# Optimization experiments

Measured on AMD Instinct MI355X. Metric: run time of the kernel, lower is better.

## Reference

```python
import jax, jax.numpy as jnp
import numpy as np

N_EMBD = 1024
N_HEAD = 16
HEAD_DIM = 64


def setup_inputs() -> dict:
    key = jax.random.key(0)
    ks = jax.random.split(key, 5)
    x = jax.random.normal(ks[0], (4, 2048, N_EMBD), dtype=jnp.float32)
    # qkv_proj: Linear(n_embd, 3*n_embd) -- torch weight is [out, in]
    W_qkv = jax.random.normal(ks[1], (3 * N_EMBD, N_EMBD), dtype=jnp.float32) * 0.02
    b_qkv = jnp.zeros((3 * N_EMBD,), dtype=jnp.float32)
    W_out = jax.random.normal(ks[2], (N_EMBD, N_EMBD), dtype=jnp.float32) * 0.02
    b_out = jnp.zeros((N_EMBD,), dtype=jnp.float32)
    return {"x": x, "W_qkv": W_qkv, "b_qkv": b_qkv, "W_out": W_out, "b_out": b_out}


def reference(x, W_qkv, b_qkv, W_out, b_out):
    B, S, C = x.shape
    scale = 1.0 / np.sqrt(HEAD_DIM)
    qkv = jnp.einsum('bsc,oc->bso', x, W_qkv) + b_qkv  # [B,S,3C]
    q, k, v = jnp.split(qkv, 3, axis=-1)
    # [B,S,C] -> [B,H,S,Dh]
    def to_heads(t):
        return t.reshape(B, S, N_HEAD, HEAD_DIM).transpose(0, 2, 1, 3)
    q, k, v = to_heads(q), to_heads(k), to_heads(v)
    scores = jnp.einsum('bhqd,bhkd->bhqk', q, k) * scale  # [B,H,S,S]
    causal = jnp.tril(jnp.ones((S, S), dtype=bool))
    scores = jnp.where(causal[None, None], scores, -jnp.inf)
    weights = jax.nn.softmax(scores.astype(jnp.float32), axis=-1).astype(q.dtype)
    y = jnp.einsum('bhqk,bhkd->bhqd', weights, v)  # [B,H,S,Dh]
    y = y.transpose(0, 2, 1, 3).reshape(B, S, C)
    return jnp.einsum('bsc,oc->bso', y, W_out) + b_out
```

## Files before the change

### kernel.cpp

```cpp
#include <hip/hip_runtime.h>
#include <stdint.h>
#include <stddef.h>

typedef __attribute__((ext_vector_type(8))) short short8;
typedef __attribute__((ext_vector_type(4))) float f32x4;
typedef __attribute__((ext_vector_type(16))) float f32x16;
typedef __attribute__((ext_vector_type(4))) unsigned short ushort4v;
typedef __attribute__((ext_vector_type(4))) unsigned int uint4v;

#define SEQ   2048
#define NH    16
#define BATCH 4
#define GK    1024

__device__ __forceinline__ unsigned short f2bf(float f) {
  union { float f; unsigned int u; } v; v.f = f;
  unsigned int u = v.u;
  u += 0x7fffu + ((u >> 16) & 1u);
  return (unsigned short)(u >> 16);
}

__device__ __forceinline__ unsigned cvtpk_bf16(float lo, float hi) {
  unsigned r;
  asm("v_cvt_pk_bf16_f32 %0, %1, %2" : "=v"(r) : "v"(lo), "v"(hi));
  return r;
}

__device__ __forceinline__ void plswap(unsigned &x, unsigned &y) {
#if __has_builtin(__builtin_amdgcn_permlane32_swap)
  auto r = __builtin_amdgcn_permlane32_swap((int)x, (int)y, false, false);
  x = (unsigned)r[0]; y = (unsigned)r[1];
#else
  const unsigned sx = (unsigned)__shfl_xor((int)x, 32);
  const unsigned sy = (unsigned)__shfl_xor((int)y, 32);
  const bool hi = (threadIdx.x & 63) >= 32;
  const unsigned nx = hi ? sy : x;
  const unsigned ny = hi ? y : sx;
  x = nx; y = ny;
#endif
}

__device__ __forceinline__ void gload16(const unsigned short* g, unsigned short* l) {
  __builtin_amdgcn_global_load_lds(
      (const __attribute__((address_space(1))) unsigned int*)g,
      (__attribute__((address_space(3))) unsigned int*)l, 16, 0, 0);
}

__global__ void cvt_all(const float* __restrict__ x, const float* __restrict__ wqkv,
                        const float* __restrict__ wout, unsigned short* __restrict__ dst) {
  const int N1 = (8192 * 1024) / 4, N2 = (3072 * 1024) / 4, N3 = (1024 * 1024) / 4;
  int i = blockIdx.x * blockDim.x + threadIdx.x;
  const int stride = gridDim.x * blockDim.x;
  for (; i < N1 + N2 + N3; i += stride) {
    float4 v;
    if (i < N1)            v = reinterpret_cast<const float4*>(x)[i];
    else if (i < N1 + N2)  v = reinterpret_cast<const float4*>(wqkv)[i - N1];
    else                   v = reinterpret_cast<const float4*>(wout)[i - N1 - N2];
    ushort4v o;
    o[0] = f2bf(v.x); o[1] = f2bf(v.y); o[2] = f2bf(v.z); o[3] = f2bf(v.w);
    reinterpret_cast<ushort4v*>(dst)[i] = o;
  }
}

template<int MODE>
__global__ __launch_bounds__(256, 3)
void gemm_bt(const unsigned short* __restrict__ A,
             const unsigned short* __restrict__ Bw,
             const float* __restrict__ bias,
             unsigned short* __restrict__ q_ws,
             unsigned short* __restrict__ k_ws,
             unsigned short* __restrict__ v_ws,
             float* __restrict__ fout,
             int N)
{
  __shared__ __attribute__((aligned(16))) unsigned short As[128 * 64];
  __shared__ __attribute__((aligned(16))) unsigned short Bs[128 * 64];

  const int t = threadIdx.x;
  const int w = t >> 6, lane = t & 63;
  const int g = lane >> 4, c = lane & 15;
  const int wrow = w >> 1, wcol = w & 1;
  const int m0 = blockIdx.y * 128;
  const int n0 = blockIdx.x * 128;

  const int r8 = lane >> 3;
  const int cgs = (lane & 7) ^ r8;

  const f32x4 fz = {0.f, 0.f, 0.f, 0.f};
  f32x4 acc[4][4];
#pragma unroll
  for (int i = 0; i < 4; ++i)
#pragma unroll
    for (int j = 0; j < 4; ++j) acc[i][j] = fz;

  for (int ks = 0; ks < GK; ks += 64) {
    __syncthreads();
#pragma unroll
    for (int i = 0; i < 4; ++i) {
      const int RB = (i * 4 + w) * 8;
      gload16(A + (size_t)(m0 + RB + r8) * GK + ks + cgs * 8, &As[RB * 64]);
      gload16(Bw + (size_t)(n0 + RB + r8) * GK + ks + cgs * 8, &Bs[RB * 64]);
    }
    __syncthreads();
#pragma unroll
    for (int kk = 0; kk < 2; ++kk) {
      short8 af[4], bfr[4];
#pragma unroll
      for (int mi = 0; mi < 4; ++mi) {
        const int row = wrow * 64 + mi * 16 + c;
        af[mi] = *reinterpret_cast<const short8*>(&As[row * 64 + (((kk * 4 + g) ^ (row & 7)) << 3)]);
      }
#pragma unroll
      for (int ni = 0; ni < 4; ++ni) {
        const int row = wcol * 64 + ni * 16 + c;
        bfr[ni] = *reinterpret_cast<const short8*>(&Bs[row * 64 + (((kk * 4 + g) ^ (row & 7)) << 3)]);
      }
#pragma unroll
      for (int mi = 0; mi < 4; ++mi)
#pragma unroll
        for (int ni = 0; ni < 4; ++ni)
          acc[mi][ni] = __builtin_amdgcn_mfma_f32_16x16x32_bf16(af[mi], bfr[ni], acc[mi][ni], 0, 0, 0);
    }
  }

  if (MODE == 0) {
    const int sec = n0 >> 10;
    unsigned short* dst = (sec == 0) ? q_ws : ((sec == 1) ? k_ws : v_ws);
    const float qsc = (sec == 0) ? (0.125f * 1.44269504f) : 1.0f;
#pragma unroll
    for (int ni = 0; ni < 4; ++ni) {
      const int n = n0 + wcol * 64 + ni * 16 + c;
      const float bb = bias[n];
      const int hh = (n & 1023) >> 6;
      const int d = n & 63;
#pragma unroll
      for (int mi = 0; mi < 4; ++mi) {
#pragma unroll
        for (int r = 0; r < 4; ++r) {
          const int m = m0 + wrow * 64 + mi * 16 + g * 4 + r;
          const int b = m >> 11, s = m & 2047;
          const float val = (acc[mi][ni][r] + bb) * qsc;
          dst[((size_t)((b * NH + hh) * SEQ + s) << 6) + d] = f2bf(val);
        }
      }
    }
  } else {
#pragma unroll
    for (int ni = 0; ni < 4; ++ni) {
      const int n = n0 + wcol * 64 + ni * 16 + c;
      const float bb = bias[n];
#pragma unroll
      for (int mi = 0; mi < 4; ++mi) {
#pragma unroll
        for (int r = 0; r < 4; ++r) {
          const int m = m0 + wrow * 64 + mi * 16 + g * 4 + r;
          fout[(size_t)m * N + n] = acc[mi][ni][r] + bb;
        }
      }
    }
  }
}

__global__ __launch_bounds__(256)
void transpose_v(const unsigned short* __restrict__ v, unsigned short* __restrict__ vt) {
  __shared__ unsigned short T[64][72];
  const int t = threadIdx.x;
  const int bh = blockIdx.y, s0 = blockIdx.x * 64;
  const unsigned short* src = v + ((size_t)bh * SEQ + s0) * 64;
#pragma unroll
  for (int rep = 0; rep < 2; ++rep) {
    const int u = rep * 256 + t;
    const int sr = u >> 3, cg = u & 7;
    const short8 x = *reinterpret_cast<const short8*>(src + (size_t)sr * 64 + cg * 8);
    *reinterpret_cast<short8*>(&T[sr][cg * 8]) = x;
  }
  __syncthreads();
  unsigned short* dst = vt + (size_t)bh * 64 * SEQ + s0;
#pragma unroll
  for (int rep = 0; rep < 2; ++rep) {
    const int u = rep * 256 + t;
    const int d = u >> 3, sc8 = u & 7;
    short8 x;
#pragma unroll
    for (int j = 0; j < 8; ++j) x[j] = (short)T[sc8 * 8 + j][d];
    *reinterpret_cast<short8*>(dst + (size_t)d * SEQ + sc8 * 8) = x;
  }
}

__global__ __launch_bounds__(512, 4)
void attn_fwd6(const unsigned short* __restrict__ q_ws,
               const unsigned short* __restrict__ k_ws,
               const unsigned short* __restrict__ vt_ws,
               unsigned short* __restrict__ y_ws)
{
  __shared__ __attribute__((aligned(16))) unsigned short Ks[2][64 * 64];
  __shared__ __attribute__((aligned(16))) unsigned short Vs[3][64 * 64];

  const int t = threadIdx.x;
  const int w = t >> 6, lane = t & 63;
  const int ql = lane & 31, hi = lane >> 5;
  const int bh = blockIdx.y, b = bh >> 4, h = bh & 15;
  const int jt = (blockIdx.y >= 32) ? (7 - (int)blockIdx.x) : (int)blockIdx.x;
  const int wq0 = jt * 256 + w * 32;
  const int nkt = 4 * jt + 4;

  const int s_row = t >> 3;
  const int s_swz = (t & 7) ^ (s_row & 7);

  const unsigned short* kbase = k_ws + (size_t)bh * SEQ * 64;
  const unsigned short* vbase = vt_ws + (size_t)bh * 64 * SEQ;

  auto stage = [&](int kt, int kb, int vb) {
    gload16(kbase + (size_t)kt * 4096 + s_row * 64 + s_swz * 8, &Ks[kb][w * 512]);
    gload16(vbase + (size_t)s_row * SEQ + kt * 64 + s_swz * 8, &Vs[vb][w * 512]);
  };

  const unsigned short* qr = q_ws + ((size_t)bh * SEQ + (wq0 + ql)) * 64;
  short8 qf[4];
#pragma unroll
  for (int ks = 0; ks < 4; ++ks)
    qf[ks] = *reinterpret_cast<const short8*>(qr + ks * 16 + hi * 8);

  f32x16 o0, o1;
#pragma unroll
  for (int i = 0; i < 16; ++i) { o0[i] = 0.f; o1[i] = 0.f; }
  float m_run = -1e30f, lsum = 0.f;
  short8 pa[4];

  stage(0, 0, 0);

#pragma unroll 1
  for (int kt = 0; kt < nkt; ++kt) {
    __syncthreads();
    if (kt + 1 < nkt) stage(kt + 1, (kt + 1) & 1, (kt + 1) % 3);
    const int cur = kt & 1;
    const int pvb = (kt + 2) % 3;
    const int kt64 = kt * 64;
    const bool act  = (kt64 <= wq0 + 31);
    const bool actp = (kt > 0) && (kt64 - 64 <= wq0 + 31);

    f32x16 s0, s1;
    if (act) {
#pragma unroll
      for (int i = 0; i < 16; ++i) { s0[i] = 0.f; s1[i] = 0.f; }
      __builtin_amdgcn_s_setprio(1);
#pragma unroll
      for (int ks = 0; ks < 4; ++ks) {
        const short8 kfl = *reinterpret_cast<const short8*>(
            &Ks[cur][ql * 64 + (((2 * ks + hi) ^ (ql & 7)) << 3)]);
        const short8 kfh = *reinterpret_cast<const short8*>(
            &Ks[cur][(32 + ql) * 64 + (((2 * ks + hi) ^ (ql & 7)) << 3)]);
        s0 = __builtin_amdgcn_mfma_f32_32x32x16_bf16(kfl, qf[ks], s0, 0, 0, 0);
        s1 = __builtin_amdgcn_mfma_f32_32x32x16_bf16(kfh, qf[ks], s1, 0, 0, 0);
      }
      __builtin_amdgcn_s_setprio(0);
    }
    if (actp) {
      __builtin_amdgcn_s_setprio(1);
#pragma unroll
      for (int ks = 0; ks < 4; ++ks) {
        const short8 vfl = *reinterpret_cast<const short8*>(
            &Vs[pvb][ql * 64 + (((2 * ks + hi) ^ (ql & 7)) << 3)]);
        const short8 vfh = *reinterpret_cast<const short8*>(
            &Vs[pvb][(32 + ql) * 64 + (((2 * ks + hi) ^ (ql & 7)) << 3)]);
        o0 = __builtin_amdgcn_mfma_f32_32x32x16_bf16(pa[ks], vfl, o0, 0, 0, 0);
        o1 = __builtin_amdgcn_mfma_f32_32x32x16_bf16(pa[ks], vfh, o1, 0, 0, 0);
      }
      __builtin_amdgcn_s_setprio(0);
    }
    if (act) {
      if (kt64 + 63 > wq0) {
        const int gq = wq0 + ql;
#pragma unroll
        for (int r = 0; r < 16; ++r) {
          const int krow = (r & 3) + 8 * (r >> 2) + 4 * hi;
          if (kt64 + krow > gq)      s0[r] = -1e30f;
          if (kt64 + 32 + krow > gq) s1[r] = -1e30f;
        }
      }
      float tm = -1e30f;
#pragma unroll
      for (int r = 0; r < 16; ++r) tm = fmaxf(tm, fmaxf(s0[r], s1[r]));
      tm = fmaxf(tm, __shfl_xor(tm, 32));
      if (__any(tm > m_run + 10.0f)) {
        const float m_new = fmaxf(m_run, tm);
        const float al = __builtin_amdgcn_exp2f(m_run - m_new);
        m_run = m_new;
        lsum *= al;
#pragma unroll
        for (int r = 0; r < 16; ++r) {
          const int qq = (r & 3) + 8 * (r >> 2) + 4 * hi;
          const float ar = __shfl(al, qq);
          o0[r] *= ar; o1[r] *= ar;
        }
      }
      float psum = 0.f;
      unsigned W[16];
#pragma unroll
      for (int half = 0; half < 2; ++half) {
#pragma unroll
        for (int gr = 0; gr < 4; ++gr) {
          const float v0 = (half ? s1[gr * 4 + 0] : s0[gr * 4 + 0]) - m_run;
          const float v1 = (half ? s1[gr * 4 + 1] : s0[gr * 4 + 1]) - m_run;
          const float v2 = (half ? s1[gr * 4 + 2] : s0[gr * 4 + 2]) - m_run;
          const float v3 = (half ? s1[gr * 4 + 3] : s0[gr * 4 + 3]) - m_run;
          const float p0 = __builtin_amdgcn_exp2f(v0);
          const float p1 = __builtin_amdgcn_exp2f(v1);
          const float p2 = __builtin_amdgcn_exp2f(v2);
          const float p3 = __builtin_amdgcn_exp2f(v3);
          psum += (p0 + p1) + (p2 + p3);
          W[half * 8 + 2 * gr]     = cvtpk_bf16(p0, p1);
          W[half * 8 + 2 * gr + 1] = cvtpk_bf16(p2, p3);
        }
      }
      lsum += psum;
#pragma unroll
      for (int q4 = 0; q4 < 4; ++q4) {
        unsigned a0 = W[q4 * 4 + 0], a1 = W[q4 * 4 + 2];
        unsigned b0 = W[q4 * 4 + 1], b1 = W[q4 * 4 + 3];
        plswap(a0, a1);
        plswap(b0, b1);
        uint4v pk; pk[0] = a0; pk[1] = b0; pk[2] = a1; pk[3] = b1;
        pa[q4] = __builtin_bit_cast(short8, pk);
      }
    }
  }

  if ((nkt - 1) * 64 <= wq0 + 31) {
    const int pvb = (nkt - 1) % 3;
    __builtin_amdgcn_s_setprio(1);
#pragma unroll
    for (int ks = 0; ks < 4; ++ks) {
      const short8 vfl = *reinterpret_cast<const short8*>(
          &Vs[pvb][ql * 64 + (((2 * ks + hi) ^ (ql & 7)) << 3)]);
      const short8 vfh = *reinterpret_cast<const short8*>(
          &Vs[pvb][(32 + ql) * 64 + (((2 * ks + hi) ^ (ql & 7)) << 3)]);
      o0 = __builtin_amdgcn_mfma_f32_32x32x16_bf16(pa[ks], vfl, o0, 0, 0, 0);
      o1 = __builtin_amdgcn_mfma_f32_32x32x16_bf16(pa[ks], vfh, o1, 0, 0, 0);
    }
    __builtin_amdgcn_s_setprio(0);
  }

  lsum += __shfl_xor(lsum, 32);
  const float linv = 1.f / lsum;
#pragma unroll
  for (int r = 0; r < 16; ++r) {
    const int qq = (r & 3) + 8 * (r >> 2) + 4 * hi;
    const float lr = __shfl(linv, qq);
    const size_t rowo = ((size_t)b * SEQ + (wq0 + qq)) * 1024 + h * 64;
    y_ws[rowo + ql]      = f2bf(o0[r] * lr);
    y_ws[rowo + 32 + ql] = f2bf(o1[r] * lr);
  }
}

extern "C" void kernel_launch(void* const* d_in, const int* in_sizes, int n_in,
                              void* d_out, int out_size, void* d_ws, size_t ws_size,
                              hipStream_t stream)
{
  (void)in_sizes; (void)n_in; (void)out_size; (void)ws_size;
  const float* x     = (const float*)d_in[0];
  const float* W_qkv = (const float*)d_in[1];
  const float* b_qkv = (const float*)d_in[2];
  const float* W_out = (const float*)d_in[3];
  const float* b_out = (const float*)d_in[4];
  float* out = (float*)d_out;

  unsigned short* ws      = (unsigned short*)d_ws;
  unsigned short* x_bf    = ws;
  unsigned short* wqkv_bf = x_bf    + (size_t)8192 * 1024;
  unsigned short* wout_bf = wqkv_bf + (size_t)3072 * 1024;
  unsigned short* q_ws    = wout_bf + (size_t)1024 * 1024;
  unsigned short* k_ws    = q_ws    + (size_t)64 * SEQ * 64;
  unsigned short* v_ws    = k_ws    + (size_t)64 * SEQ * 64;
  unsigned short* y_ws    = v_ws    + (size_t)64 * SEQ * 64;
  unsigned short* vt_ws   = x_bf;

  cvt_all<<<2048, 256, 0, stream>>>(x, W_qkv, W_out, x_bf);

  gemm_bt<0><<<dim3(24, 64), 256, 0, stream>>>(x_bf, wqkv_bf, b_qkv, q_ws, k_ws, v_ws, nullptr, 3072);
  transpose_v<<<dim3(SEQ / 64, 64), 256, 0, stream>>>(v_ws, vt_ws);
  attn_fwd6<<<dim3(8, 64), 512, 0, stream>>>(q_ws, k_ws, vt_ws, y_ws);
  gemm_bt<1><<<dim3(8, 64), 256, 0, stream>>>(y_ws, wout_bf, b_out, nullptr, nullptr, nullptr, out, 1024);
}
```

Before: 183.3 us.

## Process 128-key tiles per iteration and drop the deferred PV software pipeline

The attention kernel now stages 128-key K and V^T tiles, double-buffered, instead of 64-key tiles with a triple-buffered V. QK^T, softmax and PV all run in the same iteration, replacing the previous scheme where PV for tile kt-1 overlapped QK for tile kt. Causal masking is done per 32-key sub-block, and fully masked sub-blocks skip their MFMAs. This halves the number of barriers and loop iterations, at the cost of more LDS per block, higher register pressure (four score accumulators plus eight P fragments), and the loss of overlap between the exp work and the PV matrix multiplies.

New measurement: 358.6 us. 1.96x slower.

```diff
diff --git a/kernel.cpp b/kernel.cpp
--- a/kernel.cpp
+++ b/kernel.cpp
@@ -188,13 +188,13 @@
 }
 
 __global__ __launch_bounds__(512, 4)
-void attn_fwd6(const unsigned short* __restrict__ q_ws,
+void attn_fwd9(const unsigned short* __restrict__ q_ws,
                const unsigned short* __restrict__ k_ws,
                const unsigned short* __restrict__ vt_ws,
                unsigned short* __restrict__ y_ws)
 {
-  __shared__ __attribute__((aligned(16))) unsigned short Ks[2][64 * 64];
-  __shared__ __attribute__((aligned(16))) unsigned short Vs[3][64 * 64];
+  __shared__ __attribute__((aligned(16))) unsigned short Ks[2][128 * 64];
+  __shared__ __attribute__((aligned(16))) unsigned short Vs[2][64 * 128];
 
   const int t = threadIdx.x;
   const int w = t >> 6, lane = t & 63;
@@ -202,17 +202,23 @@
   const int bh = blockIdx.y, b = bh >> 4, h = bh & 15;
   const int jt = (blockIdx.y >= 32) ? (7 - (int)blockIdx.x) : (int)blockIdx.x;
   const int wq0 = jt * 256 + w * 32;
-  const int nkt = 4 * jt + 4;
-
-  const int s_row = t >> 3;
-  const int s_swz = (t & 7) ^ (s_row & 7);
+  const int nit = 2 * jt + 2;
 
   const unsigned short* kbase = k_ws + (size_t)bh * SEQ * 64;
   const unsigned short* vbase = vt_ws + (size_t)bh * 64 * SEQ;
 
-  auto stage = [&](int kt, int kb, int vb) {
-    gload16(kbase + (size_t)kt * 4096 + s_row * 64 + s_swz * 8, &Ks[kb][w * 512]);
-    gload16(vbase + (size_t)s_row * SEQ + kt * 64 + s_swz * 8, &Vs[vb][w * 512]);
+  const int kr0 = w * 8 + (lane >> 3);
+  const int kcs = ((lane & 7) ^ (kr0 & 7)) << 3;
+  const int vd0 = w * 4 + (lane >> 4);
+  const int vcs = ((lane & 15) ^ (vd0 & 7)) << 3;
+
+  auto stage = [&](int it, int bi) {
+    const unsigned short* kp = kbase + (size_t)it * 128 * 64;
+    gload16(kp + (size_t)kr0 * 64 + kcs, &Ks[bi][w * 512]);
+    gload16(kp + (size_t)(kr0 + 64) * 64 + kcs, &Ks[bi][64 * 64 + w * 512]);
+    const unsigned short* vp = vbase + (size_t)it * 128;
+    gload16(vp + (size_t)vd0 * SEQ + vcs, &Vs[bi][w * 512]);
+    gload16(vp + (size_t)(vd0 + 32) * SEQ + vcs, &Vs[bi][32 * 128 + w * 512]);
   };
 
   const unsigned short* qr = q_ws + ((size_t)bh * SEQ + (wq0 + ql)) * 64;
@@ -225,62 +231,91 @@
 #pragma unroll
   for (int i = 0; i < 16; ++i) { o0[i] = 0.f; o1[i] = 0.f; }
   float m_run = -1e30f, lsum = 0.f;
-  short8 pa[4];
-
-  stage(0, 0, 0);
+
+  stage(0, 0);
 
 #pragma unroll 1
-  for (int kt = 0; kt < nkt; ++kt) {
+  for (int it = 0; it < nit; ++it) {
     __syncthreads();
-    if (kt + 1 < nkt) stage(kt + 1, (kt + 1) & 1, (kt + 1) % 3);
-    const int cur = kt & 1;
-    const int pvb = (kt + 2) % 3;
-    const int kt64 = kt * 64;
-    const bool act  = (kt64 <= wq0 + 31);
-    const bool actp = (kt > 0) && (kt64 - 64 <= wq0 + 31);
-
-    f32x16 s0, s1;
-    if (act) {
-#pragma unroll
-      for (int i = 0; i < 16; ++i) { s0[i] = 0.f; s1[i] = 0.f; }
+    if (it + 1 < nit) stage(it + 1, (it + 1) & 1);
+    const int cur = it & 1;
+    const int it128 = it * 128;
+
+    if (it128 <= wq0 + 31) {
+      const bool a1 = (it128 + 32 <= wq0 + 31);
+      const bool a2 = (it128 + 64 <= wq0 + 31);
+      const bool a3 = (it128 + 96 <= wq0 + 31);
+
+      f32x16 s0, s1, s2, s3;
+#pragma unroll
+      for (int i = 0; i < 16; ++i) { s0[i] = 0.f; s1[i] = 0.f; s2[i] = 0.f; s3[i] = 0.f; }
+      const int cq = (ql & 7) ;
       __builtin_amdgcn_s_setprio(1);
 #pragma unroll
       for (int ks = 0; ks < 4; ++ks) {
-        const short8 kfl = *reinterpret_cast<const short8*>(
-            &Ks[cur][ql * 64 + (((2 * ks + hi) ^ (ql & 7)) << 3)]);
-        const short8 kfh = *reinterpret_cast<const short8*>(
-            &Ks[cur][(32 + ql) * 64 + (((2 * ks + hi) ^ (ql & 7)) << 3)]);
-        s0 = __builtin_amdgcn_mfma_f32_32x32x16_bf16(kfl, qf[ks], s0, 0, 0, 0);
-        s1 = __builtin_amdgcn_mfma_f32_32x32x16_bf16(kfh, qf[ks], s1, 0, 0, 0);
+        const int co = ((2 * ks + hi) ^ cq) << 3;
+        const short8 k0 = *reinterpret_cast<const short8*>(&Ks[cur][(ql) * 64 + co]);
+        s0 = __builtin_amdgcn_mfma_f32_32x32x16_bf16(k0, qf[ks], s0, 0, 0, 0);
+        if (a1) {
+          const short8 k1 = *reinterpret_cast<const short8*>(&Ks[cur][(32 + ql) * 64 + co]);
+          s1 = __builtin_amdgcn_mfma_f32_32x32x16_bf16(k1, qf[ks], s1, 0, 0, 0);
+        }
+        if (a2) {
+          const short8 k2 = *reinterpret_cast<const short8*>(&Ks[cur][(64 + ql) * 64 + co]);
+          s2 = __builtin_amdgcn_mfma_f32_32x32x16_bf16(k2, qf[ks], s2, 0, 0, 0);
+        }
+        if (a3) {
+          const short8 k3 = *reinterpret_cast<const short8*>(&Ks[cur][(96 + ql) * 64 + co]);
+          s3 = __builtin_amdgcn_mfma_f32_32x32x16_bf16(k3, qf[ks], s3, 0, 0, 0);
+        }
       }
       __builtin_amdgcn_s_setprio(0);
-    }
-    if (actp) {
-      __builtin_amdgcn_s_setprio(1);
-#pragma unroll
-      for (int ks = 0; ks < 4; ++ks) {
-        const short8 vfl = *reinterpret_cast<const short8*>(
-            &Vs[pvb][ql * 64 + (((2 * ks + hi) ^ (ql & 7)) << 3)]);
-        const short8 vfh = *reinterpret_cast<const short8*>(
-            &Vs[pvb][(32 + ql) * 64 + (((2 * ks + hi) ^ (ql & 7)) << 3)]);
-        o0 = __builtin_amdgcn_mfma_f32_32x32x16_bf16(pa[ks], vfl, o0, 0, 0, 0);
-        o1 = __builtin_amdgcn_mfma_f32_32x32x16_bf16(pa[ks], vfh, o1, 0, 0, 0);
-      }
-      __builtin_amdgcn_s_setprio(0);
-    }
-    if (act) {
-      if (kt64 + 63 > wq0) {
-        const int gq = wq0 + ql;
+
+      const int gq = wq0 + ql;
+      if (it128 + 31 > wq0) {
 #pragma unroll
         for (int r = 0; r < 16; ++r) {
-          const int krow = (r & 3) + 8 * (r >> 2) + 4 * hi;
-          if (kt64 + krow > gq)      s0[r] = -1e30f;
-          if (kt64 + 32 + krow > gq) s1[r] = -1e30f;
-        }
-      }
+          const int key = it128 + (r & 3) + 8 * (r >> 2) + 4 * hi;
+          if (key > gq) s0[r] = -1e30f;
+        }
+      }
+      if (a1 && it128 + 63 > wq0) {
+#pragma unroll
+        for (int r = 0; r < 16; ++r) {
+          const int key = it128 + 32 + (r & 3) + 8 * (r >> 2) + 4 * hi;
+          if (key > gq) s1[r] = -1e30f;
+        }
+      }
+      if (a2 && it128 + 95 > wq0) {
+#pragma unroll
+        for (int r = 0; r < 16; ++r) {
+          const int key = it128 + 64 + (r & 3) + 8 * (r >> 2) + 4 * hi;
+          if (key > gq) s2[r] = -1e30f;
+        }
+      }
+      if (a3 && it128 + 127 > wq0) {
+#pragma unroll
+        for (int r = 0; r < 16; ++r) {
+          const int key = it128 + 96 + (r & 3) + 8 * (r >> 2) + 4 * hi;
+          if (key > gq) s3[r] = -1e30f;
+        }
+      }
+
       float tm = -1e30f;
 #pragma unroll
-      for (int r = 0; r < 16; ++r) tm = fmaxf(tm, fmaxf(s0[r], s1[r]));
+      for (int r = 0; r < 16; ++r) tm = fmaxf(tm, s0[r]);
+      if (a1) {
+#pragma unroll
+        for (int r = 0; r < 16; ++r) tm = fmaxf(tm, s1[r]);
+      }
+      if (a2) {
+#pragma unroll
+        for (int r = 0; r < 16; ++r) tm = fmaxf(tm, s2[r]);
+      }
+      if (a3) {
+#pragma unroll
+        for (int r = 0; r < 16; ++r) tm = fmaxf(tm, s3[r]);
+      }
       tm = fmaxf(tm, __shfl_xor(tm, 32));
       if (__any(tm > m_run + 10.0f)) {
         const float m_new = fmaxf(m_run, tm);
@@ -294,51 +329,50 @@
           o0[r] *= ar; o1[r] *= ar;
         }
       }
+
       float psum = 0.f;
-      unsigned W[16];
-#pragma unroll
-      for (int half = 0; half < 2; ++half) {
+      short8 pa[8];
+      auto packsb = [&](const f32x16& s, short8& pA, short8& pB) {
+        unsigned W8[8];
 #pragma unroll
         for (int gr = 0; gr < 4; ++gr) {
-          const float v0 = (half ? s1[gr * 4 + 0] : s0[gr * 4 + 0]) - m_run;
-          const float v1 = (half ? s1[gr * 4 + 1] : s0[gr * 4 + 1]) - m_run;
-          const float v2 = (half ? s1[gr * 4 + 2] : s0[gr * 4 + 2]) - m_run;
-          const float v3 = (half ? s1[gr * 4 + 3] : s0[gr * 4 + 3]) - m_run;
-          const float p0 = __builtin_amdgcn_exp2f(v0);
-          const float p1 = __builtin_amdgcn_exp2f(v1);
-          const float p2 = __builtin_amdgcn_exp2f(v2);
-          const float p3 = __builtin_amdgcn_exp2f(v3);
+          const float p0 = __builtin_amdgcn_exp2f(s[gr * 4 + 0] - m_run);
+          const float p1 = __builtin_amdgcn_exp2f(s[gr * 4 + 1] - m_run);
+          const float p2 = __builtin_amdgcn_exp2f(s[gr * 4 + 2] - m_run);
+          const float p3 = __builtin_amdgcn_exp2f(s[gr * 4 + 3] - m_run);
           psum += (p0 + p1) + (p2 + p3);
-          W[half * 8 + 2 * gr]     = cvtpk_bf16(p0, p1);
-          W[half * 8 + 2 * gr + 1] = cvtpk_bf16(p2, p3);
-        }
-      }
+          W8[2 * gr]     = cvtpk_bf16(p0, p1);
+          W8[2 * gr + 1] = cvtpk_bf16(p2, p3);
+        }
+        unsigned x0 = W8[0], x1 = W8[2], y0 = W8[1], y1 = W8[3];
+        plswap(x0, x1); plswap(y0, y1);
+        uint4v pk0; pk0[0] = x0; pk0[1] = y0; pk0[2] = x1; pk0[3] = y1;
+        pA = __builtin_bit_cast(short8, pk0);
+        x0 = W8[4]; x1 = W8[6]; y0 = W8[5]; y1 = W8[7];
+        plswap(x0, x1); plswap(y0, y1);
+        uint4v pk1; pk1[0] = x0; pk1[1] = y0; pk1[2] = x1; pk1[3] = y1;
+        pB = __builtin_bit_cast(short8, pk1);
+      };
+      packsb(s0, pa[0], pa[1]);
+      if (a1) packsb(s1, pa[2], pa[3]);
+      if (a2) packsb(s2, pa[4], pa[5]);
+      if (a3) packsb(s3, pa[6], pa[7]);
       lsum += psum;
-#pragma unroll
-      for (int q4 = 0; q4 < 4; ++q4) {
-        unsigned a0 = W[q4 * 4 + 0], a1 = W[q4 * 4 + 2];
-        unsigned b0 = W[q4 * 4 + 1], b1 = W[q4 * 4 + 3];
-        plswap(a0, a1);
-        plswap(b0, b1);
-        uint4v pk; pk[0] = a0; pk[1] = b0; pk[2] = a1; pk[3] = b1;
-        pa[q4] = __builtin_bit_cast(short8, pk);
-      }
+
+      __builtin_amdgcn_s_setprio(1);
+#pragma unroll
+      for (int ks = 0; ks < 8; ++ks) {
+        const bool actk = (ks < 2) || (ks < 4 && a1) || (ks < 6 && a2) || a3;
+        if (actk) {
+          const int co = ((2 * ks + hi) ^ cq) << 3;
+          const short8 vf0 = *reinterpret_cast<const short8*>(&Vs[cur][ql * 128 + co]);
+          const short8 vf1 = *reinterpret_cast<const short8*>(&Vs[cur][(32 + ql) * 128 + co]);
+          o0 = __builtin_amdgcn_mfma_f32_32x32x16_bf16(pa[ks], vf0, o0, 0, 0, 0);
+          o1 = __builtin_amdgcn_mfma_f32_32x32x16_bf16(pa[ks], vf1, o1, 0, 0, 0);
+        }
+      }
+      __builtin_amdgcn_s_setprio(0);
     }
-  }
-
-  if ((nkt - 1) * 64 <= wq0 + 31) {
-    const int pvb = (nkt - 1) % 3;
-    __builtin_amdgcn_s_setprio(1);
-#pragma unroll
-    for (int ks = 0; ks < 4; ++ks) {
-      const short8 vfl = *reinterpret_cast<const short8*>(
-          &Vs[pvb][ql * 64 + (((2 * ks + hi) ^ (ql & 7)) << 3)]);
-      const short8 vfh = *reinterpret_cast<const short8*>(
-          &Vs[pvb][(32 + ql) * 64 + (((2 * ks + hi) ^ (ql & 7)) << 3)]);
-      o0 = __builtin_amdgcn_mfma_f32_32x32x16_bf16(pa[ks], vfl, o0, 0, 0, 0);
-      o1 = __builtin_amdgcn_mfma_f32_32x32x16_bf16(pa[ks], vfh, o1, 0, 0, 0);
-    }
-    __builtin_amdgcn_s_setprio(0);
   }
 
   lsum += __shfl_xor(lsum, 32);
@@ -379,6 +413,6 @@
 
   gemm_bt<0><<<dim3(24, 64), 256, 0, stream>>>(x_bf, wqkv_bf, b_qkv, q_ws, k_ws, v_ws, nullptr, 3072);
   transpose_v<<<dim3(SEQ / 64, 64), 256, 0, stream>>>(v_ws, vt_ws);
-  attn_fwd6<<<dim3(8, 64), 512, 0, stream>>>(q_ws, k_ws, vt_ws, y_ws);
+  attn_fwd9<<<dim3(8, 64), 512, 0, stream>>>(q_ws, k_ws, vt_ws, y_ws);
   gemm_bt<1><<<dim3(8, 64), 256, 0, stream>>>(y_ws, wout_bf, b_out, nullptr, nullptr, nullptr, out, 1024);
 }
```
